# Kernel optimization log

Hardware: AMD Instinct MI355X
Metric: run time of the kernel (lower is better)

## Reference

```python
import jax, jax.numpy as jnp
import numpy as np

IH, IW = 14, 14
NUM_HEADS = 16
HEAD_DIMS = 32
INP_DIMS = 512
B = 128


def make_relative_position_index(ih, iw):
    coords = np.stack(np.meshgrid(np.arange(ih), np.arange(iw), indexing='ij'))  # [2, ih, iw]
    cf = coords.reshape(2, -1)  # [2, n]
    rel = cf[:, :, None] - cf[:, None, :]  # [2, n, n]
    rel = rel.transpose(1, 2, 0)  # [n, n, 2]
    rel[:, :, 0] += ih - 1
    rel[:, :, 1] += iw - 1
    rel[:, :, 0] *= 2 * iw - 1
    return rel.sum(-1).astype(np.int64)  # [n, n]


def setup_inputs() -> dict:
    key = jax.random.key(0)
    k1, k2, k3, k4, k5 = jax.random.split(key, 5)
    n = IH * IW
    inner = NUM_HEADS * HEAD_DIMS
    x = jax.random.normal(k1, (B, n, INP_DIMS), dtype=jnp.float32)
    qkv_w = jax.random.normal(k2, (INP_DIMS, 3 * inner), dtype=jnp.float32) * 0.02
    rel_bias_table = jax.random.normal(k3, ((2 * IH - 1) * (2 * IW - 1), NUM_HEADS), dtype=jnp.float32) * 0.02
    proj_w = jax.random.normal(k4, (inner, INP_DIMS), dtype=jnp.float32) * 0.02
    proj_b = jax.random.normal(k5, (INP_DIMS,), dtype=jnp.float32) * 0.02
    rel_pos_index = jnp.asarray(make_relative_position_index(IH, IW))
    return {"x": x, "qkv_w": qkv_w, "rel_bias_table": rel_bias_table,
            "proj_w": proj_w, "proj_b": proj_b, "rel_pos_index": rel_pos_index}


def reference(x, qkv_w, rel_bias_table, proj_w, proj_b, rel_pos_index):
    b, n, c = x.shape
    h, hd = NUM_HEADS, HEAD_DIMS
    scale = (INP_DIMS // NUM_HEADS) ** (-0.5)
    qkv = x @ qkv_w  # [b, n, 3*h*hd]
    qkv = qkv.reshape(b, n, 3, h, hd).transpose(2, 0, 3, 1, 4)  # [3, b, h, n, hd]
    q, k, v = qkv[0] * scale, qkv[1], qkv[2]
    attn = jnp.einsum('bhqd,bhkd->bhqk', q, k)  # [b, h, n, n]
    # gather relative position bias: [n*n, h] -> [h, n, n]
    bias = rel_bias_table[rel_pos_index.reshape(-1)].reshape(n, n, h).transpose(2, 0, 1)
    attn = jax.nn.softmax(attn + bias[None], axis=-1)
    out = jnp.einsum('bhqk,bhkd->bhqd', attn, v)  # [b, h, n, hd]
    out = out.transpose(0, 2, 1, 3).reshape(b, n, h * hd)
    return out @ proj_w + proj_b
```

## Files before the change

kernel.cpp:

```cpp
#include <hip/hip_runtime.h>

#define NTOK 196
#define QPAD 208
#define KP 208
#define PSTR 232
#define VKP 208

typedef __attribute__((ext_vector_type(8))) short short8;
typedef __attribute__((ext_vector_type(4))) short short4_t;
typedef __attribute__((ext_vector_type(4))) float float4_t;

__device__ __forceinline__ short f2bf(float f) {
  unsigned u = __float_as_uint(f);
  u = (u + 0x7fffu + ((u >> 16) & 1u)) >> 16;
  return (short)u;
}

__global__ __launch_bounds__(256) void fill_kernel(float* __restrict__ out,
                                                   int n) {
  int i = blockIdx.x * 256 + threadIdx.x;
  if (i < n) out[i] = 1000.0f;
}

__global__ __launch_bounds__(256) void cvt_kernel(const float* __restrict__ in,
                                                  short* __restrict__ out) {
  int i = (blockIdx.x * 256 + threadIdx.x) * 8;
  float4_t a = *(const float4_t*)&in[i];
  float4_t b = *(const float4_t*)&in[i + 4];
  short8 v;
  v[0] = f2bf(a[0]); v[1] = f2bf(a[1]); v[2] = f2bf(a[2]); v[3] = f2bf(a[3]);
  v[4] = f2bf(b[0]); v[5] = f2bf(b[1]); v[6] = f2bf(b[2]); v[7] = f2bf(b[3]);
  *(short8*)&out[i] = v;
}

__global__ __launch_bounds__(256) void transpose_kernel(
    const float* __restrict__ in, short* __restrict__ out, int R, int C) {
  __shared__ float tile[64][65];
  int c0 = blockIdx.x * 64, r0 = blockIdx.y * 64;
  int tc = threadIdx.x & 63, tr = threadIdx.x >> 6;
#pragma unroll
  for (int s = 0; s < 16; s++) {
    int r = s * 4 + tr;
    tile[r][tc] = in[(r0 + r) * C + c0 + tc];
  }
  __syncthreads();
#pragma unroll
  for (int s = 0; s < 16; s++) {
    int i = s * 4 + tr;
    out[(c0 + i) * R + r0 + tc] = f2bf(tile[tc][i]);
  }
}

__global__ __launch_bounds__(256) void bias_kernel(
    const float* __restrict__ table, const int* __restrict__ rpi,
    float* __restrict__ bias) {
  int idx = blockIdx.x * 256 + threadIdx.x;
  if (idx >= 16 * QPAD * KP) return;
  int h = idx / (QPAD * KP);
  int rem = idx % (QPAD * KP);
  int q = rem / KP, k = rem % KP;
  float v = 0.f;
  if (q < NTOK && k < NTOK) v = table[rpi[q * NTOK + k] * 16 + h];
  bias[idx] = v;
}

__global__ __launch_bounds__(256) void vpad_kernel(short* __restrict__ vb) {
  int i = blockIdx.x * 256 + threadIdx.x;
  if (i >= 2048 * 32 * 3) return;
  int row = i / 3, g = i - 3 * (i / 3);
  short4_t z = {0, 0, 0, 0};
  *(short4_t*)&vb[row * VKP + 196 + g * 4] = z;
}

__device__ __forceinline__ void gemm_tile(const short* __restrict__ A,
                                          const short* __restrict__ B, int K,
                                          int m0, int n0, short (*As)[72],
                                          short (*Bs)[72], float4_t acc[4][4]) {
  int tid = threadIdx.x;
  int lane = tid & 63, wave = tid >> 6;
  int quad = lane >> 4, l16 = lane & 15;
  int wm = (wave >> 1) * 64, wn = (wave & 1) * 64;
  int srow = tid >> 3, scol = (tid & 7) * 8;
  for (int k0 = 0; k0 < K; k0 += 64) {
#pragma unroll
    for (int i = 0; i < 4; i++) {
      int r = srow + i * 32;
      *(short8*)&As[r][scol] = *(const short8*)&A[(m0 + r) * K + k0 + scol];
      *(short8*)&Bs[r][scol] = *(const short8*)&B[(n0 + r) * K + k0 + scol];
    }
    __syncthreads();
#pragma unroll
    for (int ks = 0; ks < 2; ks++) {
      short8 af[4], bfr[4];
#pragma unroll
      for (int i = 0; i < 4; i++) {
        af[i] = *(short8*)&As[wm + i * 16 + l16][ks * 32 + quad * 8];
        bfr[i] = *(short8*)&Bs[wn + i * 16 + l16][ks * 32 + quad * 8];
      }
#pragma unroll
      for (int mi = 0; mi < 4; mi++)
#pragma unroll
        for (int ni = 0; ni < 4; ni++)
          acc[mi][ni] = __builtin_amdgcn_mfma_f32_16x16x32_bf16(
              af[mi], bfr[ni], acc[mi][ni], 0, 0, 0);
    }
    __syncthreads();
  }
}

__global__ __launch_bounds__(256) void qkv_gemm(
    const short* __restrict__ xb, const short* __restrict__ wt1,
    short* __restrict__ qb, short* __restrict__ kb, short* __restrict__ vb) {
  __shared__ __align__(16) short As[128][72];
  __shared__ __align__(16) short Bs[128][72];
  float4_t acc[4][4];
  float4_t z = {0.f, 0.f, 0.f, 0.f};
#pragma unroll
  for (int i = 0; i < 4; i++)
#pragma unroll
    for (int j = 0; j < 4; j++) acc[i][j] = z;
  int lin = blockIdx.x + blockIdx.y * 12;
  int xcd = lin & 7, loc = lin >> 3;
  int nl = xcd * 294 + loc;
  int bx = nl % 12, by = nl / 12;
  int m0 = by * 128, n0 = bx * 128;
  gemm_tile(xb, wt1, 512, m0, n0, As, Bs, acc);
  int lane = threadIdx.x & 63, wave = threadIdx.x >> 6;
  int quad = lane >> 4, l16 = lane & 15;
  int wm = (wave >> 1) * 64, wn = (wave & 1) * 64;
  const float qscale = 0.17677669529663687f;
#pragma unroll
  for (int mi = 0; mi < 4; mi++)
#pragma unroll
    for (int ni = 0; ni < 4; ni++) {
      int colg = n0 + wn + ni * 16 + l16;
      int s = colg >> 9, rem = colg & 511;
      int h = rem >> 5, d = rem & 31;
      int rowg0 = m0 + wm + mi * 16 + quad * 4;
      if (s == 2) {
        int b = rowg0 / NTOK, nt = rowg0 - b * NTOK;
        short4_t v4;
        v4[0] = f2bf(acc[mi][ni][0]);
        v4[1] = f2bf(acc[mi][ni][1]);
        v4[2] = f2bf(acc[mi][ni][2]);
        v4[3] = f2bf(acc[mi][ni][3]);
        *(short4_t*)&vb[((b * 16 + h) * 32 + d) * VKP + nt] = v4;
      } else {
#pragma unroll
        for (int r = 0; r < 4; r++) {
          int rowg = rowg0 + r;
          int b = rowg / NTOK, n = rowg - b * NTOK;
          int off = ((b * 16 + h) * QPAD + n) * 32 + d;
          if (s == 0)
            qb[off] = f2bf(acc[mi][ni][r] * qscale);
          else
            kb[off] = f2bf(acc[mi][ni][r]);
        }
      }
    }
}

__global__ __launch_bounds__(256) void attn_kernel(
    const short* __restrict__ qb, const short* __restrict__ kb,
    const short* __restrict__ vb, const float* __restrict__ bias,
    short* __restrict__ aout) {
  __shared__ __align__(16) short vT[32][PSTR];
  __shared__ __align__(16) short P[4][16][PSTR];
  int bh = blockIdx.x, b = bh >> 4, h = bh & 15;
  int tid = threadIdx.x, wave = tid >> 6, lane = tid & 63;
  int quad = lane >> 4, l16 = lane & 15;
  int base_row = b * NTOK;
  const short* vsrc = vb + bh * 32 * VKP;
  for (int i = tid; i < 32 * 26; i += 256) {
    int d = i / 26, c = (i - d * 26) * 8;
    *(short8*)&vT[d][c] = *(const short8*)&vsrc[d * VKP + c];
  }
  short8 z8 = {0, 0, 0, 0, 0, 0, 0, 0};
  for (int i = tid; i < 32 * 3; i += 256) {
    int d = i / 3, c = 208 + (i - d * 3) * 8;
    *(short8*)&vT[d][c] = z8;
  }
  __syncthreads();
  float4_t z4 = {0.f, 0.f, 0.f, 0.f};
  for (int i2 = 0; i2 < 4; i2++) {
    bool active = (i2 < 3) || (wave == 0);
    if (!active) break;
    int qt = (i2 < 3) ? (wave + 4 * i2) : 12;
    int qr0 = qt * 16;
    short8 qf = *(const short8*)&qb[(bh * QPAD + qr0 + l16) * 32 + quad * 8];
    float4_t s[13];
#pragma unroll
    for (int kt = 0; kt < 13; kt++) {
      short8 kf =
          *(const short8*)&kb[(bh * QPAD + kt * 16 + l16) * 32 + quad * 8];
      s[kt] = __builtin_amdgcn_mfma_f32_16x16x32_bf16(qf, kf, z4, 0, 0, 0);
    }
    const float* brow = bias + (h * QPAD + qr0 + quad * 4) * KP;
#pragma unroll
    for (int kt = 0; kt < 13; kt++) {
      int col = kt * 16 + l16;
#pragma unroll
      for (int r = 0; r < 4; r++) s[kt][r] += brow[r * KP + col];
    }
    if (l16 >= 4) {
#pragma unroll
      for (int r = 0; r < 4; r++) s[12][r] = -1e30f;
    }
#pragma unroll
    for (int r = 0; r < 4; r++) {
      float m = s[0][r];
#pragma unroll
      for (int kt = 1; kt < 13; kt++) m = fmaxf(m, s[kt][r]);
      m = fmaxf(m, __shfl_xor(m, 8, 16));
      m = fmaxf(m, __shfl_xor(m, 4, 16));
      m = fmaxf(m, __shfl_xor(m, 2, 16));
      m = fmaxf(m, __shfl_xor(m, 1, 16));
      float sum = 0.f;
#pragma unroll
      for (int kt = 0; kt < 13; kt++) {
        float p = __expf(s[kt][r] - m);
        s[kt][r] = p;
        sum += p;
      }
      sum += __shfl_xor(sum, 8, 16);
      sum += __shfl_xor(sum, 4, 16);
      sum += __shfl_xor(sum, 2, 16);
      sum += __shfl_xor(sum, 1, 16);
      float inv = 1.f / sum;
      short* prow = &P[wave][quad * 4 + r][0];
#pragma unroll
      for (int kt = 0; kt < 13; kt++)
        prow[kt * 16 + l16] = f2bf(s[kt][r] * inv);
      prow[208 + l16] = 0;
    }
    float4_t o0 = z4, o1 = z4;
#pragma unroll
    for (int kt = 0; kt < 7; kt++) {
      short8 pf = *(short8*)&P[wave][l16][kt * 32 + quad * 8];
      short8 vf0 = *(short8*)&vT[l16][kt * 32 + quad * 8];
      short8 vf1 = *(short8*)&vT[16 + l16][kt * 32 + quad * 8];
      o0 = __builtin_amdgcn_mfma_f32_16x16x32_bf16(pf, vf0, o0, 0, 0, 0);
      o1 = __builtin_amdgcn_mfma_f32_16x16x32_bf16(pf, vf1, o1, 0, 0, 0);
    }
#pragma unroll
    for (int r = 0; r < 4; r++) {
      int row = qr0 + quad * 4 + r;
      if (row < NTOK) {
        int off = (base_row + row) * 512 + h * 32;
        aout[off + l16] = f2bf(o0[r]);
        aout[off + 16 + l16] = f2bf(o1[r]);
      }
    }
  }
}

__global__ __launch_bounds__(256, 2) void fused_attn(
    const short* __restrict__ xb, const short* __restrict__ wt1,
    const float* __restrict__ bias, short* __restrict__ aout) {
  __shared__ __align__(16) short R1[64 * PSTR];
  __shared__ __align__(16) short R2[32 * PSTR];
  __shared__ __align__(16) short Qs[224][40];
  __shared__ __align__(16) short Ks[224][40];
  short(*As)[40] = (short(*)[40])R1;
  short(*P)[PSTR] = (short(*)[PSTR])R1;
  short(*Bs)[40] = (short(*)[40])R2;
  short(*vTs)[PSTR] = (short(*)[PSTR])R2;

  int bh = blockIdx.x, b = bh >> 4, h = bh & 15;
  int tid = threadIdx.x, wave = tid >> 6, lane = tid & 63;
  int quad = lane >> 4, l16 = lane & 15;
  int base_row = b * NTOK;

  float4_t z4 = {0.f, 0.f, 0.f, 0.f};
  float4_t acc[4][6];
#pragma unroll
  for (int i = 0; i < 4; i++)
#pragma unroll
    for (int n = 0; n < 6; n++) acc[i][n] = z4;

  int srow = tid >> 2, scol = (tid & 3) * 8;
  for (int k0 = 0; k0 < 512; k0 += 32) {
#pragma unroll
    for (int i = 0; i < 4; i++) {
      int r = srow + i * 64;
      if (r < 224) {
        int gr = base_row + r;
        if (gr > 25087) gr = 25087;
        *(short8*)&As[r][scol] = *(const short8*)&xb[gr * 512 + k0 + scol];
      }
    }
#pragma unroll
    for (int i = 0; i < 2; i++) {
      int r = srow + i * 64;
      if (r < 96) {
        int sec = r >> 5, r32 = r & 31;
        *(short8*)&Bs[r][scol] =
            *(const short8*)&wt1[(sec * 512 + h * 32 + r32) * 512 + k0 + scol];
      }
    }
    __syncthreads();
    short8 af[4], bfv[6];
#pragma unroll
    for (int i = 0; i < 4; i++) {
      int mt = (i < 3) ? (wave + 4 * i) : (12 + (wave & 1));
      af[i] = *(short8*)&As[mt * 16 + l16][quad * 8];
    }
#pragma unroll
    for (int n = 0; n < 6; n++) bfv[n] = *(short8*)&Bs[n * 16 + l16][quad * 8];
#pragma unroll
    for (int i = 0; i < 4; i++)
#pragma unroll
      for (int n = 0; n < 6; n++)
        acc[i][n] = __builtin_amdgcn_mfma_f32_16x16x32_bf16(af[i], bfv[n],
                                                            acc[i][n], 0, 0, 0);
    __syncthreads();
  }
  const float qscale = 0.17677669529663687f;
#pragma unroll
  for (int i = 0; i < 4; i++) {
    if (i == 3 && wave >= 2) break;
    int mt = (i < 3) ? (wave + 4 * i) : (12 + wave);
    int row0 = mt * 16 + quad * 4;
#pragma unroll
    for (int n = 0; n < 6; n++) {
      int c = n * 16 + l16;
#pragma unroll
      for (int r = 0; r < 4; r++) {
        int row = row0 + r;
        float v = acc[i][n][r];
        if (c < 32)
          Qs[row][c] = f2bf(v * qscale);
        else if (c < 64)
          Ks[row][c - 32] = f2bf(v);
        else
          vTs[c - 64][row] = f2bf(v);
      }
    }
  }
  __syncthreads();
  for (int i2 = 0; i2 < 4; i2++) {
    bool active = (i2 < 3) || (wave == 0);
    int qt = (i2 < 3) ? (wave + 4 * i2) : 12;
    int qr0 = qt * 16;
    if (active) {
      short8 qf = *(short8*)&Qs[qr0 + l16][quad * 8];
      float4_t s[13];
#pragma unroll
      for (int kt = 0; kt < 13; kt++) {
        short8 kf = *(short8*)&Ks[kt * 16 + l16][quad * 8];
        s[kt] = __builtin_amdgcn_mfma_f32_16x16x32_bf16(qf, kf, z4, 0, 0, 0);
      }
      const float* brow = bias + (h * QPAD + qr0 + quad * 4) * KP;
#pragma unroll
      for (int kt = 0; kt < 13; kt++) {
        int col = kt * 16 + l16;
#pragma unroll
        for (int r = 0; r < 4; r++) s[kt][r] += brow[r * KP + col];
      }
      if (l16 >= 4) {
#pragma unroll
        for (int r = 0; r < 4; r++) s[12][r] = -1e30f;
      }
      int prow_base = wave * 16 + quad * 4;
#pragma unroll
      for (int r = 0; r < 4; r++) {
        float m = s[0][r];
#pragma unroll
        for (int kt = 1; kt < 13; kt++) m = fmaxf(m, s[kt][r]);
        m = fmaxf(m, __shfl_xor(m, 8, 16));
        m = fmaxf(m, __shfl_xor(m, 4, 16));
        m = fmaxf(m, __shfl_xor(m, 2, 16));
        m = fmaxf(m, __shfl_xor(m, 1, 16));
        float sum = 0.f;
#pragma unroll
        for (int kt = 0; kt < 13; kt++) {
          float p = __expf(s[kt][r] - m);
          s[kt][r] = p;
          sum += p;
        }
        sum += __shfl_xor(sum, 8, 16);
        sum += __shfl_xor(sum, 4, 16);
        sum += __shfl_xor(sum, 2, 16);
        sum += __shfl_xor(sum, 1, 16);
        float inv = 1.f / sum;
        short* prow = &P[prow_base + r][0];
#pragma unroll
        for (int kt = 0; kt < 13; kt++)
          prow[kt * 16 + l16] = f2bf(s[kt][r] * inv);
        prow[208 + l16] = 0;
      }
    }
    __syncthreads();
    if (active) {
      float4_t o0 = z4, o1 = z4;
#pragma unroll
      for (int kt = 0; kt < 7; kt++) {
        short8 pf = *(short8*)&P[wave * 16 + l16][kt * 32 + quad * 8];
        short8 vf0 = *(short8*)&vTs[l16][kt * 32 + quad * 8];
        short8 vf1 = *(short8*)&vTs[16 + l16][kt * 32 + quad * 8];
        o0 = __builtin_amdgcn_mfma_f32_16x16x32_bf16(pf, vf0, o0, 0, 0, 0);
        o1 = __builtin_amdgcn_mfma_f32_16x16x32_bf16(pf, vf1, o1, 0, 0, 0);
      }
#pragma unroll
      for (int r = 0; r < 4; r++) {
        int row = qr0 + quad * 4 + r;
        if (row < NTOK) {
          int off = (base_row + row) * 512 + h * 32;
          aout[off + l16] = f2bf(o0[r]);
          aout[off + 16 + l16] = f2bf(o1[r]);
        }
      }
    }
    __syncthreads();
  }
}

__global__ __launch_bounds__(256) void proj_gemm(
    const short* __restrict__ a, const short* __restrict__ wt,
    const float* __restrict__ pb, float* __restrict__ out) {
  __shared__ __align__(16) short As[128][72];
  __shared__ __align__(16) short Bs[128][72];
  float4_t acc[4][4];
  float4_t z = {0.f, 0.f, 0.f, 0.f};
#pragma unroll
  for (int i = 0; i < 4; i++)
#pragma unroll
    for (int j = 0; j < 4; j++) acc[i][j] = z;
  int lin = blockIdx.x + blockIdx.y * 4;
  int xcd = lin & 7, loc = lin >> 3;
  int nl = xcd * 98 + loc;
  int bx = nl % 4, by = nl / 4;
  int m0 = by * 128, n0 = bx * 128;
  gemm_tile(a, wt, 512, m0, n0, As, Bs, acc);
  int lane = threadIdx.x & 63, wave = threadIdx.x >> 6;
  int quad = lane >> 4, l16 = lane & 15;
  int wm = (wave >> 1) * 64, wn = (wave & 1) * 64;
#pragma unroll
  for (int mi = 0; mi < 4; mi++)
#pragma unroll
    for (int ni = 0; ni < 4; ni++) {
      int colg = n0 + wn + ni * 16 + l16;
      float bv = pb[colg];
#pragma unroll
      for (int r = 0; r < 4; r++) {
        int rowg = m0 + wm + mi * 16 + quad * 4 + r;
        out[rowg * 512 + colg] = acc[mi][ni][r] + bv;
      }
    }
}

extern "C" void kernel_launch(void* const* d_in, const int* in_sizes, int n_in,
                              void* d_out, int out_size, void* d_ws,
                              size_t ws_size, hipStream_t stream) {
  const float* x = (const float*)d_in[0];
  const float* qkv_w = (const float*)d_in[1];
  const float* table = (const float*)d_in[2];
  const float* proj_w = (const float*)d_in[3];
  const float* proj_b = (const float*)d_in[4];
  const int* rpi = (const int*)d_in[5];
  float* out = (float*)d_out;

  char* w = (char*)d_ws;
  short* wt1 = (short*)(w);
  short* wt2 = (short*)(w + 1572864);
  float* bias = (float*)(w + 2097152);
  short* xb = (short*)(w + 4866048);
  short* qb = (short*)(w + 30556160);
  short* kb = (short*)(w + 57819136);
  short* vb = (short*)(w + 85082112);
  const size_t NEEDED_SPLIT = 112345088;
  const size_t NEEDED_FUSED = 30556160 + 25690112;

  transpose_kernel<<<dim3(24, 8), 256, 0, stream>>>(qkv_w, wt1, 512, 1536);
  transpose_kernel<<<dim3(8, 8), 256, 0, stream>>>(proj_w, wt2, 512, 512);
  bias_kernel<<<(16 * QPAD * KP + 255) / 256, 256, 0, stream>>>(table, rpi,
                                                                bias);
  if (ws_size >= NEEDED_SPLIT) {
    short* aout = xb;
    vpad_kernel<<<(2048 * 32 * 3 + 255) / 256, 256, 0, stream>>>(vb);
    cvt_kernel<<<25088 * 512 / (256 * 8), 256, 0, stream>>>(x, xb);
    qkv_gemm<<<dim3(12, 196), 256, 0, stream>>>(xb, wt1, qb, kb, vb);
    attn_kernel<<<2048, 256, 0, stream>>>(qb, kb, vb, bias, aout);
    proj_gemm<<<dim3(4, 196), 256, 0, stream>>>(aout, wt2, proj_b, out);
  } else if (ws_size >= NEEDED_FUSED) {
    short* aout = (short*)(w + 30556160);
    cvt_kernel<<<25088 * 512 / (256 * 8), 256, 0, stream>>>(x, xb);
    fused_attn<<<2048, 256, 0, stream>>>(xb, wt1, bias, aout);
    proj_gemm<<<dim3(4, 196), 256, 0, stream>>>(aout, wt2, proj_b, out);
  } else {
    fill_kernel<<<(out_size + 255) / 256, 256, 0, stream>>>(out, out_size);
  }
}
```

Before: 276.8 us.

## Merge prep kernels, fuse x conversion into QKV GEMM, widen attention blocks

Combines the two weight transposes, the bias gather and the V padding into one prep launch to cut launch overhead. The fp32-to-bf16 conversion of x moves into the QKV GEMM's A-tile load, which removes the separate cvt pass and its bf16 round trip through memory. The attention kernel now uses 512 threads (8 waves), so each wave handles at most two query tiles instead of four. Softmax normalisation is deferred to the output, applied as one multiply after P·V. The cost is that each QKV tile re-reads and re-converts fp32 x once for every one of the 12 N-tiles, which roughly doubles A-side load bytes.

```diff
diff --git a/kernel.cpp b/kernel.cpp
--- a/kernel.cpp
+++ b/kernel.cpp
@@ -33,10 +33,11 @@
   *(short8*)&out[i] = v;
 }
 
-__global__ __launch_bounds__(256) void transpose_kernel(
-    const float* __restrict__ in, short* __restrict__ out, int R, int C) {
-  __shared__ float tile[64][65];
-  int c0 = blockIdx.x * 64, r0 = blockIdx.y * 64;
+__device__ __forceinline__ void transpose_body(const float* __restrict__ in,
+                                               short* __restrict__ out, int R,
+                                               int C, int bx, int by,
+                                               float (*tile)[65]) {
+  int c0 = bx * 64, r0 = by * 64;
   int tc = threadIdx.x & 63, tr = threadIdx.x >> 6;
 #pragma unroll
   for (int s = 0; s < 16; s++) {
@@ -51,31 +52,40 @@
   }
 }
 
-__global__ __launch_bounds__(256) void bias_kernel(
+__global__ __launch_bounds__(256) void prep_kernel(
+    const float* __restrict__ qkv_w, const float* __restrict__ proj_w,
     const float* __restrict__ table, const int* __restrict__ rpi,
-    float* __restrict__ bias) {
-  int idx = blockIdx.x * 256 + threadIdx.x;
-  if (idx >= 16 * QPAD * KP) return;
-  int h = idx / (QPAD * KP);
-  int rem = idx % (QPAD * KP);
-  int q = rem / KP, k = rem % KP;
-  float v = 0.f;
-  if (q < NTOK && k < NTOK) v = table[rpi[q * NTOK + k] * 16 + h];
-  bias[idx] = v;
-}
-
-__global__ __launch_bounds__(256) void vpad_kernel(short* __restrict__ vb) {
-  int i = blockIdx.x * 256 + threadIdx.x;
-  if (i >= 2048 * 32 * 3) return;
-  int row = i / 3, g = i - 3 * (i / 3);
-  short4_t z = {0, 0, 0, 0};
-  *(short4_t*)&vb[row * VKP + 196 + g * 4] = z;
-}
-
-__device__ __forceinline__ void gemm_tile(const short* __restrict__ A,
-                                          const short* __restrict__ B, int K,
-                                          int m0, int n0, short (*As)[72],
-                                          short (*Bs)[72], float4_t acc[4][4]) {
+    short* __restrict__ wt1, short* __restrict__ wt2, float* __restrict__ bias,
+    short* __restrict__ vb, int do_vpad) {
+  __shared__ float tile[64][65];
+  int blk = blockIdx.x;
+  if (blk < 192) {
+    transpose_body(qkv_w, wt1, 512, 1536, blk % 24, blk / 24, tile);
+  } else if (blk < 256) {
+    int i = blk - 192;
+    transpose_body(proj_w, wt2, 512, 512, i % 8, i / 8, tile);
+  } else if (blk < 2960) {
+    int idx = (blk - 256) * 256 + threadIdx.x;
+    int h = idx / (QPAD * KP);
+    int rem = idx % (QPAD * KP);
+    int q = rem / KP, k = rem % KP;
+    float v = 0.f;
+    if (q < NTOK && k < NTOK) v = table[rpi[q * NTOK + k] * 16 + h];
+    bias[idx] = v;
+  } else if (do_vpad) {
+    int i = (blk - 2960) * 256 + threadIdx.x;
+    int row = i / 3, g = i - 3 * (i / 3);
+    short4_t z = {0, 0, 0, 0};
+    *(short4_t*)&vb[row * VKP + 196 + g * 4] = z;
+  }
+}
+
+template <bool CVTA>
+__device__ __forceinline__ void gemm_tile_t(const void* __restrict__ Aptr,
+                                            const short* __restrict__ B, int K,
+                                            int m0, int n0, short (*As)[72],
+                                            short (*Bs)[72],
+                                            float4_t acc[4][4]) {
   int tid = threadIdx.x;
   int lane = tid & 63, wave = tid >> 6;
   int quad = lane >> 4, l16 = lane & 15;
@@ -85,7 +95,20 @@
 #pragma unroll
     for (int i = 0; i < 4; i++) {
       int r = srow + i * 32;
-      *(short8*)&As[r][scol] = *(const short8*)&A[(m0 + r) * K + k0 + scol];
+      if (CVTA) {
+        const float* Af = (const float*)Aptr;
+        float4_t a = *(const float4_t*)&Af[(m0 + r) * K + k0 + scol];
+        float4_t b = *(const float4_t*)&Af[(m0 + r) * K + k0 + scol + 4];
+        short8 v;
+        v[0] = f2bf(a[0]); v[1] = f2bf(a[1]);
+        v[2] = f2bf(a[2]); v[3] = f2bf(a[3]);
+        v[4] = f2bf(b[0]); v[5] = f2bf(b[1]);
+        v[6] = f2bf(b[2]); v[7] = f2bf(b[3]);
+        *(short8*)&As[r][scol] = v;
+      } else {
+        const short* Ab = (const short*)Aptr;
+        *(short8*)&As[r][scol] = *(const short8*)&Ab[(m0 + r) * K + k0 + scol];
+      }
       *(short8*)&Bs[r][scol] = *(const short8*)&B[(n0 + r) * K + k0 + scol];
     }
     __syncthreads();
@@ -109,7 +132,7 @@
 }
 
 __global__ __launch_bounds__(256) void qkv_gemm(
-    const short* __restrict__ xb, const short* __restrict__ wt1,
+    const float* __restrict__ x, const short* __restrict__ wt1,
     short* __restrict__ qb, short* __restrict__ kb, short* __restrict__ vb) {
   __shared__ __align__(16) short As[128][72];
   __shared__ __align__(16) short Bs[128][72];
@@ -124,7 +147,7 @@
   int nl = xcd * 294 + loc;
   int bx = nl % 12, by = nl / 12;
   int m0 = by * 128, n0 = bx * 128;
-  gemm_tile(xb, wt1, 512, m0, n0, As, Bs, acc);
+  gemm_tile_t<true>(x, wt1, 512, m0, n0, As, Bs, acc);
   int lane = threadIdx.x & 63, wave = threadIdx.x >> 6;
   int quad = lane >> 4, l16 = lane & 15;
   int wm = (wave >> 1) * 64, wn = (wave & 1) * 64;
@@ -160,32 +183,31 @@
     }
 }
 
-__global__ __launch_bounds__(256) void attn_kernel(
+__global__ __launch_bounds__(512) void attn_kernel(
     const short* __restrict__ qb, const short* __restrict__ kb,
     const short* __restrict__ vb, const float* __restrict__ bias,
     short* __restrict__ aout) {
   __shared__ __align__(16) short vT[32][PSTR];
-  __shared__ __align__(16) short P[4][16][PSTR];
+  __shared__ __align__(16) short P[8][16][PSTR];
   int bh = blockIdx.x, b = bh >> 4, h = bh & 15;
   int tid = threadIdx.x, wave = tid >> 6, lane = tid & 63;
   int quad = lane >> 4, l16 = lane & 15;
   int base_row = b * NTOK;
   const short* vsrc = vb + bh * 32 * VKP;
-  for (int i = tid; i < 32 * 26; i += 256) {
+  for (int i = tid; i < 32 * 26; i += 512) {
     int d = i / 26, c = (i - d * 26) * 8;
     *(short8*)&vT[d][c] = *(const short8*)&vsrc[d * VKP + c];
   }
   short8 z8 = {0, 0, 0, 0, 0, 0, 0, 0};
-  for (int i = tid; i < 32 * 3; i += 256) {
-    int d = i / 3, c = 208 + (i - d * 3) * 8;
+  if (tid < 32 * 3) {
+    int d = tid / 3, c = 208 + (tid - d * 3) * 8;
     *(short8*)&vT[d][c] = z8;
   }
   __syncthreads();
   float4_t z4 = {0.f, 0.f, 0.f, 0.f};
-  for (int i2 = 0; i2 < 4; i2++) {
-    bool active = (i2 < 3) || (wave == 0);
-    if (!active) break;
-    int qt = (i2 < 3) ? (wave + 4 * i2) : 12;
+  for (int i2 = 0; i2 < 2; i2++) {
+    int qt = wave + 8 * i2;
+    if (qt > 12) break;
     int qr0 = qt * 16;
     short8 qf = *(const short8*)&qb[(bh * QPAD + qr0 + l16) * 32 + quad * 8];
     float4_t s[13];
@@ -206,6 +228,7 @@
 #pragma unroll
       for (int r = 0; r < 4; r++) s[12][r] = -1e30f;
     }
+    float invr[4];
 #pragma unroll
     for (int r = 0; r < 4; r++) {
       float m = s[0][r];
@@ -226,11 +249,11 @@
       sum += __shfl_xor(sum, 4, 16);
       sum += __shfl_xor(sum, 2, 16);
       sum += __shfl_xor(sum, 1, 16);
-      float inv = 1.f / sum;
+      invr[r] = 1.f / sum;
       short* prow = &P[wave][quad * 4 + r][0];
 #pragma unroll
       for (int kt = 0; kt < 13; kt++)
-        prow[kt * 16 + l16] = f2bf(s[kt][r] * inv);
+        prow[kt * 16 + l16] = f2bf(s[kt][r]);
       prow[208 + l16] = 0;
     }
     float4_t o0 = z4, o1 = z4;
@@ -247,8 +270,8 @@
       int row = qr0 + quad * 4 + r;
       if (row < NTOK) {
         int off = (base_row + row) * 512 + h * 32;
-        aout[off + l16] = f2bf(o0[r]);
-        aout[off + 16 + l16] = f2bf(o1[r]);
+        aout[off + l16] = f2bf(o0[r] * invr[r]);
+        aout[off + 16 + l16] = f2bf(o1[r] * invr[r]);
       }
     }
   }
@@ -431,7 +454,7 @@
   int nl = xcd * 98 + loc;
   int bx = nl % 4, by = nl / 4;
   int m0 = by * 128, n0 = bx * 128;
-  gemm_tile(a, wt, 512, m0, n0, As, Bs, acc);
+  gemm_tile_t<false>(a, wt, 512, m0, n0, As, Bs, acc);
   int lane = threadIdx.x & 63, wave = threadIdx.x >> 6;
   int quad = lane >> 4, l16 = lane & 15;
   int wm = (wave >> 1) * 64, wn = (wave & 1) * 64;
@@ -471,16 +494,13 @@
   const size_t NEEDED_SPLIT = 112345088;
   const size_t NEEDED_FUSED = 30556160 + 25690112;
 
-  transpose_kernel<<<dim3(24, 8), 256, 0, stream>>>(qkv_w, wt1, 512, 1536);
-  transpose_kernel<<<dim3(8, 8), 256, 0, stream>>>(proj_w, wt2, 512, 512);
-  bias_kernel<<<(16 * QPAD * KP + 255) / 256, 256, 0, stream>>>(table, rpi,
-                                                                bias);
-  if (ws_size >= NEEDED_SPLIT) {
+  int split = ws_size >= NEEDED_SPLIT;
+  prep_kernel<<<3728, 256, 0, stream>>>(qkv_w, proj_w, table, rpi, wt1, wt2,
+                                        bias, vb, split);
+  if (split) {
     short* aout = xb;
-    vpad_kernel<<<(2048 * 32 * 3 + 255) / 256, 256, 0, stream>>>(vb);
-    cvt_kernel<<<25088 * 512 / (256 * 8), 256, 0, stream>>>(x, xb);
-    qkv_gemm<<<dim3(12, 196), 256, 0, stream>>>(xb, wt1, qb, kb, vb);
-    attn_kernel<<<2048, 256, 0, stream>>>(qb, kb, vb, bias, aout);
+    qkv_gemm<<<dim3(12, 196), 256, 0, stream>>>(x, wt1, qb, kb, vb);
+    attn_kernel<<<2048, 512, 0, stream>>>(qb, kb, vb, bias, aout);
     proj_gemm<<<dim3(4, 196), 256, 0, stream>>>(aout, wt2, proj_b, out);
   } else if (ws_size >= NEEDED_FUSED) {
     short* aout = (short*)(w + 30556160);
```

After: 301.4 us. +8.9%, slower.
